# Kernel optimization log

Measured on AMD Instinct MI355X. Metric: run time of the kernel, lower is better.

The kernel has to match this reference:

```python
import jax, jax.numpy as jnp
import numpy as np

N_NODES = 65536   # N
D_HID   = 128     # D (hidden)
N_GROUPS = 16384  # G portfolios
GROUP_LEN = 64    # lines per portfolio (port_len entries)
N_LINES = N_GROUPS * GROUP_LEN  # L
BATCH = 16384     # B samples


def setup_inputs() -> dict:
    key = jax.random.key(0)
    k = jax.random.split(key, 5)
    H = jax.random.normal(k[0], (N_NODES, D_HID), dtype=jnp.float32)
    port_w_signed_flat = jax.random.normal(k[1], (N_LINES,), dtype=jnp.float32)
    anchor_idx = jax.random.randint(k[2], (BATCH,), 0, N_NODES, dtype=jnp.int32)
    pf_gid = jax.random.randint(k[3], (BATCH,), 0, N_GROUPS, dtype=jnp.int32)
    port_nodes_flat = jax.random.randint(k[4], (N_LINES,), 0, N_NODES, dtype=jnp.int32)
    port_len = jnp.full((N_GROUPS,), GROUP_LEN, dtype=jnp.int32)
    return {
        'H': H,
        'port_w_signed_flat': port_w_signed_flat,
        'anchor_idx': anchor_idx,
        'pf_gid': pf_gid,
        'port_nodes_flat': port_nodes_flat,
        'port_len': port_len,
    }


def reference(H, port_w_signed_flat, anchor_idx, pf_gid, port_nodes_flat, port_len):
    """Faithful, vectorized port of compute_samplewise_portfolio_vectors_loo.

    Ragged segment-weighted mean per portfolio group, with strict leave-one-out
    correction for each sample's anchor node, followed by L2 normalization.
    Returns (V_abs, V_sgn), each [B, D].
    """
    N, D = H.shape
    G = port_len.shape[0]
    L = port_nodes_flat.shape[0]

    # gid per flat line: repeat_interleave(arange(G), lens)
    gid_lines = jnp.repeat(jnp.arange(G, dtype=jnp.int32), port_len,
                           total_repeat_length=L)

    w_abs = jnp.abs(port_w_signed_flat)
    Hl = H[port_nodes_flat]                                  # [L, D] gather
    S_abs = jax.ops.segment_sum(w_abs[:, None] * Hl, gid_lines, num_segments=G)
    W_abs = jax.ops.segment_sum(w_abs, gid_lines, num_segments=G)
    W_sgn = jax.ops.segment_sum(port_w_signed_flat, gid_lines, num_segments=G)

    valid = (pf_gid >= 0) & (pf_gid < G)
    g = jnp.clip(pf_gid, 0, G - 1)

    # Leave-one-out self-weight: sum of w over lines where (gid==g_i, node==anchor_i).
    # Vectorized join via a sorted composite int32 key (G*N < 2^31 by construction).
    keys_l = gid_lines * N + port_nodes_flat                 # [L]
    keys_s = g * N + anchor_idx                              # [B]
    order = jnp.argsort(keys_l)
    sk = keys_l[order]
    zero1 = jnp.zeros((1,), H.dtype)
    ca = jnp.concatenate([zero1, jnp.cumsum(w_abs[order])])
    cs = jnp.concatenate([zero1, jnp.cumsum(port_w_signed_flat[order])])
    lo = jnp.searchsorted(sk, keys_s, side='left')
    hi = jnp.searchsorted(sk, keys_s, side='right')
    self_w_abs = ca[hi] - ca[lo]                             # [B]
    self_w_sgn = cs[hi] - cs[lo]                             # [B]

    Ha = H[anchor_idx]                                       # [B, D]
    denom = jnp.maximum(W_abs[g] - self_w_abs, 1e-12)        # clamp_min
    V_abs = (S_abs[g] - self_w_abs[:, None] * Ha) / denom[:, None]
    V_sgn = ((W_sgn[g] - self_w_sgn) / denom)[:, None] * V_abs

    V_abs = jnp.where(valid[:, None], V_abs, jnp.zeros((), H.dtype))
    V_sgn = jnp.where(valid[:, None], V_sgn, jnp.zeros((), H.dtype))

    # torch F.normalize: x / clamp(||x||, min=eps)
    na = jnp.linalg.norm(V_abs, axis=1, keepdims=True)
    V_abs = V_abs / jnp.maximum(na, 1e-6)
    ns = jnp.linalg.norm(V_sgn, axis=1, keepdims=True)
    V_sgn = jnp.where(ns > 0, V_sgn / jnp.maximum(ns, 1e-6), V_sgn)
    return V_abs, V_sgn
```

## Files before the change

kernel.cpp:

```cpp
#include <hip/hip_runtime.h>
#include <hip/hip_bf16.h>


#define DDIM 128

__device__ inline unsigned bf_rne(float x) {
    unsigned u = __float_as_uint(x);
    return (u + 0x7FFFu + ((u >> 16) & 1u)) >> 16;
}

__device__ inline void unpack2(unsigned d, float& lo, float& hi) {
    lo = __uint_as_float(d << 16);
    hi = __uint_as_float(d & 0xFFFF0000u);
}

__global__ __launch_bounds__(1024) void init_kernel(
    const float4* __restrict__ H4, uint2* __restrict__ Hb, int n4,
    const int* __restrict__ plen, int* __restrict__ offs, int G,
    const int* __restrict__ pf_gid, int* __restrict__ used, int B, int nconv) {
    const int t = threadIdx.x;
    const int bb = blockIdx.x;
    if (bb < nconv) {
        const int i = bb * 1024 + t;
        if (i < n4) {
            const float4 v = H4[i];
            uint2 o;
            o.x = bf_rne(v.x) | (bf_rne(v.y) << 16);
            o.y = bf_rne(v.z) | (bf_rne(v.w) << 16);
            Hb[i] = o;
        }
        return;
    }
    if (bb == nconv) {
        for (int i = t; i < G; i += 1024) used[i] = 0;
        __syncthreads();
        for (int i = t; i < B; i += 1024) {
            const int g = pf_gid[i];
            if (g >= 0 && g < G) used[g] = 1;
        }
        return;
    }
    __shared__ int part[1024];
    const int chunk = (G + 1023) >> 10;
    const int lo = min(t * chunk, G);
    const int hi = min(lo + chunk, G);
    int s = 0;
    for (int i = lo; i < hi; ++i) s += plen[i];
    part[t] = s;
    __syncthreads();
    #pragma unroll
    for (int ofs = 1; ofs < 1024; ofs <<= 1) {
        int v = (t >= ofs) ? part[t - ofs] : 0;
        __syncthreads();
        part[t] += v;
        __syncthreads();
    }
    int run = part[t] - s;
    for (int i = lo; i < hi; ++i) { offs[i] = run; run += plen[i]; }
}

__global__ __launch_bounds__(128) void group_sums(
    const unsigned short* __restrict__ Hb,
    const float* __restrict__ pw, const int* __restrict__ pn,
    const int* __restrict__ plen, const int* __restrict__ offs,
    const int* __restrict__ used,
    float* __restrict__ Sabs, float* __restrict__ Wag,
    float* __restrict__ Wsg, int G) {
    const int g = blockIdx.x;
    if (g >= G || !used[g]) return;
    const int tid = threadIdx.x;
    const int wid = tid >> 6;
    const int lane = tid & 63;
    const int q = lane >> 4;
    const int s = lane & 15;

    __shared__ float ldsS[2][DDIM];
    __shared__ float ldsW[4];

    const int off = offs[g];
    const int len = plen[g];

    float acc[8] = {0.f, 0.f, 0.f, 0.f, 0.f, 0.f, 0.f, 0.f};
    float laWa = 0.f, laWs = 0.f;

    for (int base = 0; base < len; base += 64) {
        const int l0 = base + wid * 32;
        float wl = 0.f;
        int nl = 0;
        if (lane < 32 && l0 + lane < len) {
            wl = pw[off + l0 + lane];
            nl = pn[off + l0 + lane];
        }
        laWa += fabsf(wl);
        laWs += wl;

        #pragma unroll
        for (int jj = 0; jj < 32; jj += 4) {
            const float ww = fabsf(__shfl(wl, jj + q));
            const int row = __shfl(nl, jj + q);
            const uint4 h = *((const uint4*)(Hb + (size_t)row * DDIM) + s);
            float f0, f1, f2, f3, f4, f5, f6, f7;
            unpack2(h.x, f0, f1);
            unpack2(h.y, f2, f3);
            unpack2(h.z, f4, f5);
            unpack2(h.w, f6, f7);
            acc[0] = fmaf(ww, f0, acc[0]);
            acc[1] = fmaf(ww, f1, acc[1]);
            acc[2] = fmaf(ww, f2, acc[2]);
            acc[3] = fmaf(ww, f3, acc[3]);
            acc[4] = fmaf(ww, f4, acc[4]);
            acc[5] = fmaf(ww, f5, acc[5]);
            acc[6] = fmaf(ww, f6, acc[6]);
            acc[7] = fmaf(ww, f7, acc[7]);
        }
    }

    #pragma unroll
    for (int m = 32; m; m >>= 1) {
        laWa += __shfl_xor(laWa, m);
        laWs += __shfl_xor(laWs, m);
    }
    #pragma unroll
    for (int k = 0; k < 8; ++k) {
        acc[k] += __shfl_xor(acc[k], 16);
        acc[k] += __shfl_xor(acc[k], 32);
    }

    if (q == 0) {
        #pragma unroll
        for (int k = 0; k < 8; ++k) ldsS[wid][8 * s + k] = acc[k];
    }
    if (lane == 0) { ldsW[wid] = laWa; ldsW[2 + wid] = laWs; }
    __syncthreads();

    if (tid < DDIM) {
        Sabs[(size_t)g * DDIM + tid] = ldsS[0][tid] + ldsS[1][tid];
    }
    if (tid == 0) {
        Wag[g] = ldsW[0] + ldsW[1];
        Wsg[g] = ldsW[2] + ldsW[3];
    }
}

__global__ __launch_bounds__(256) void per_sample(
    const unsigned short* __restrict__ Hb,
    const float* __restrict__ pw, const int* __restrict__ pn,
    const int* __restrict__ plen, const int* __restrict__ offs,
    const float* __restrict__ Sabs, const float* __restrict__ Wag,
    const float* __restrict__ Wsg,
    const int* __restrict__ anchor_idx, const int* __restrict__ pf_gid,
    float* __restrict__ out, int B, int G) {
    const int b = blockIdx.x * (blockDim.x >> 6) + (threadIdx.x >> 6);
    const int lane = threadIdx.x & 63;
    if (b >= B) return;

    float2* outA = (float2*)(out + (size_t)b * DDIM);
    float2* outS = (float2*)(out + ((size_t)B + b) * DDIM);

    const int g = pf_gid[b];
    if (!(g >= 0 && g < G)) {
        const float2 z = make_float2(0.f, 0.f);
        outA[lane] = z;
        outS[lane] = z;
        return;
    }

    const int anchor = anchor_idx[b];
    const int off = offs[g];
    const int len = plen[g];

    float selfa = 0.f, selfs = 0.f;
    for (int base = 0; base < len; base += 64) {
        const int jmax = min(64, len - base);
        if (lane < jmax) {
            const float w = pw[off + base + lane];
            const int n = pn[off + base + lane];
            if (n == anchor) { selfa += fabsf(w); selfs += w; }
        }
    }
    #pragma unroll
    for (int m = 32; m; m >>= 1) {
        selfa += __shfl_xor(selfa, m);
        selfs += __shfl_xor(selfs, m);
    }

    const float Wa = Wag[g];
    const float Wsn = Wsg[g];
    const float2 S = ((const float2*)(Sabs + (size_t)g * DDIM))[lane];
    const unsigned hb = *((const unsigned*)(Hb + (size_t)anchor * DDIM) + lane);
    float h0, h1;
    unpack2(hb, h0, h1);

    const float denom = fmaxf(Wa - selfa, 1e-12f);
    float2 v;
    v.x = (S.x - selfa * h0) / denom;
    v.y = (S.y - selfa * h1) / denom;
    const float scale = (Wsn - selfs) / denom;

    float n2 = v.x * v.x + v.y * v.y;
    #pragma unroll
    for (int m = 32; m; m >>= 1) n2 += __shfl_xor(n2, m);
    const float na = sqrtf(n2);

    const float invA = 1.0f / fmaxf(na, 1e-6f);
    const float ns = fabsf(scale) * na;
    const float sgnscale = (ns > 0.f) ? (scale / fmaxf(ns, 1e-6f)) : scale;

    outA[lane] = make_float2(v.x * invA, v.y * invA);
    outS[lane] = make_float2(v.x * sgnscale, v.y * sgnscale);
}

__global__ __launch_bounds__(1024) void scan_only(
    const int* __restrict__ len, int* __restrict__ offs, int G) {
    __shared__ int part[1024];
    const int t = threadIdx.x;
    const int chunk = (G + 1023) >> 10;
    const int lo = min(t * chunk, G);
    const int hi = min(lo + chunk, G);
    int s = 0;
    for (int i = lo; i < hi; ++i) s += len[i];
    part[t] = s;
    __syncthreads();
    #pragma unroll
    for (int ofs = 1; ofs < 1024; ofs <<= 1) {
        int v = (t >= ofs) ? part[t - ofs] : 0;
        __syncthreads();
        part[t] += v;
        __syncthreads();
    }
    int run = part[t] - s;
    for (int i = lo; i < hi; ++i) { offs[i] = run; run += len[i]; }
}

__global__ __launch_bounds__(256) void pf_loo_f32(
    const float* __restrict__ H, const float* __restrict__ pw,
    const int* __restrict__ anchor_idx, const int* __restrict__ pf_gid,
    const int* __restrict__ pn, const int* __restrict__ plen,
    const int* __restrict__ offs, float* __restrict__ out, int B, int G) {
    const int b = blockIdx.x * (blockDim.x >> 6) + (threadIdx.x >> 6);
    const int lane = threadIdx.x & 63;
    const int half = lane >> 5;
    const int qlane = lane & 31;
    if (b >= B) return;
    float4* outA = (float4*)(out + (size_t)b * DDIM);
    float4* outS = (float4*)(out + ((size_t)B + b) * DDIM);
    const int gid = pf_gid[b];
    if (!(gid >= 0 && gid < G)) {
        float4 z = make_float4(0.f, 0.f, 0.f, 0.f);
        if (half == 0) { outA[qlane] = z; outS[qlane] = z; }
        return;
    }
    const int anchor = anchor_idx[b];
    const int off = offs[gid];
    const int len = plen[gid];
    float4 acc = make_float4(0.f, 0.f, 0.f, 0.f);
    float laWa = 0.f, laWs = 0.f, laSa = 0.f, laSs = 0.f;
    for (int base = 0; base < len; base += 64) {
        const int jmax = min(64, len - base);
        float wl = 0.f;
        int nl = -1;
        if (lane < jmax) { wl = pw[off + base + lane]; nl = pn[off + base + lane]; }
        const float wla = fabsf(wl);
        laWa += wla; laWs += wl;
        if (nl == anchor) { laSa += wla; laSs += wl; }
        #pragma unroll 8
        for (int jj = 0; jj < 64; jj += 2) {
            const float ww = fabsf(__shfl(wl, jj + half));
            const int row = __shfl(nl, jj + half);
            const float4 h = ((const float4*)(H + (size_t)row * DDIM))[qlane];
            acc.x = fmaf(ww, h.x, acc.x);
            acc.y = fmaf(ww, h.y, acc.y);
            acc.z = fmaf(ww, h.z, acc.z);
            acc.w = fmaf(ww, h.w, acc.w);
        }
    }
    #pragma unroll
    for (int m = 32; m; m >>= 1) {
        laWa += __shfl_xor(laWa, m);
        laWs += __shfl_xor(laWs, m);
        laSa += __shfl_xor(laSa, m);
        laSs += __shfl_xor(laSs, m);
    }
    acc.x += __shfl_xor(acc.x, 32);
    acc.y += __shfl_xor(acc.y, 32);
    acc.z += __shfl_xor(acc.z, 32);
    acc.w += __shfl_xor(acc.w, 32);
    const float denom = fmaxf(laWa - laSa, 1e-12f);
    const float4 hv = ((const float4*)(H + (size_t)anchor * DDIM))[qlane];
    float4 v;
    v.x = (acc.x - laSa * hv.x) / denom;
    v.y = (acc.y - laSa * hv.y) / denom;
    v.z = (acc.z - laSa * hv.z) / denom;
    v.w = (acc.w - laSa * hv.w) / denom;
    const float scale = (laWs - laSs) / denom;
    float n2 = v.x * v.x + v.y * v.y + v.z * v.z + v.w * v.w;
    #pragma unroll
    for (int m = 32; m; m >>= 1) n2 += __shfl_xor(n2, m);
    n2 *= 0.5f;
    const float na = sqrtf(n2);
    const float invA = 1.0f / fmaxf(na, 1e-6f);
    const float ns = fabsf(scale) * na;
    const float sgnscale = (ns > 0.f) ? (scale / fmaxf(ns, 1e-6f)) : scale;
    const float sc = half ? sgnscale : invA;
    float4 res = make_float4(v.x * sc, v.y * sc, v.z * sc, v.w * sc);
    float4* dst = half ? outS : outA;
    dst[qlane] = res;
}

extern "C" void kernel_launch(void* const* d_in, const int* in_sizes, int n_in,
                              void* d_out, int out_size, void* d_ws, size_t ws_size,
                              hipStream_t stream) {
    const float* H      = (const float*)d_in[0];
    const float* pw     = (const float*)d_in[1];
    const int* anchor   = (const int*)d_in[2];
    const int* gid      = (const int*)d_in[3];
    const int* pn       = (const int*)d_in[4];
    const int* plen     = (const int*)d_in[5];
    float* out          = (float*)d_out;

    const int B = in_sizes[2];
    const int G = in_sizes[5];
    const int ND = in_sizes[0];
    const size_t hb_bytes = (size_t)ND * 2;
    const size_t sabs_bytes = (size_t)G * DDIM * 4;
    const size_t need = hb_bytes + sabs_bytes + (size_t)G * 4 * 4;

    if (ws_size >= need) {
        char* p = (char*)d_ws;
        unsigned short* Hb = (unsigned short*)p;        p += hb_bytes;
        float* Sabs        = (float*)p;                 p += sabs_bytes;
        int* offsp         = (int*)p;                   p += (size_t)G * 4;
        int* usedp         = (int*)p;                   p += (size_t)G * 4;
        float* Wag         = (float*)p;                 p += (size_t)G * 4;
        float* Wsg         = (float*)p;

        const int n4 = ND / 4;
        const int nconv = (n4 + 1023) / 1024;
        init_kernel<<<nconv + 2, 1024, 0, stream>>>(
            (const float4*)H, (uint2*)Hb, n4, plen, offsp, G, gid, usedp, B, nconv);

        group_sums<<<G, 128, 0, stream>>>(Hb, pw, pn, plen, offsp, usedp,
                                          Sabs, Wag, Wsg, G);

        const int sblocks = (B + 3) / 4;
        per_sample<<<sblocks, 256, 0, stream>>>(Hb, pw, pn, plen, offsp, Sabs,
                                                Wag, Wsg, anchor, gid, out, B, G);
    } else {
        int* offsp = (int*)d_ws;
        scan_only<<<1, 1024, 0, stream>>>(plen, offsp, G);
        const int blocks = (B + 3) / 4;
        pf_loo_f32<<<blocks, 256, 0, stream>>>(H, pw, anchor, gid, pn, plen,
                                               offsp, out, B, G);
    }
}
```

Before: 142.9 us.

## Compute each group sum with one wavefront instead of a two-wave block

```diff
diff --git a/kernel.cpp b/kernel.cpp
--- a/kernel.cpp
+++ b/kernel.cpp
@@ -59,24 +59,20 @@
     for (int i = lo; i < hi; ++i) { offs[i] = run; run += plen[i]; }
 }
 
-__global__ __launch_bounds__(128) void group_sums(
+__global__ __launch_bounds__(256) void group_sums(
     const unsigned short* __restrict__ Hb,
     const float* __restrict__ pw, const int* __restrict__ pn,
     const int* __restrict__ plen, const int* __restrict__ offs,
     const int* __restrict__ used,
     float* __restrict__ Sabs, float* __restrict__ Wag,
     float* __restrict__ Wsg, int G) {
-    const int g = blockIdx.x;
-    if (g >= G || !used[g]) return;
-    const int tid = threadIdx.x;
-    const int wid = tid >> 6;
-    const int lane = tid & 63;
+    const int g = blockIdx.x * 4 + (threadIdx.x >> 6);
+    if (g >= G) return;
+    if (!used[g]) return;
+    const int lane = threadIdx.x & 63;
     const int q = lane >> 4;
     const int s = lane & 15;
 
-    __shared__ float ldsS[2][DDIM];
-    __shared__ float ldsW[4];
-
     const int off = offs[g];
     const int len = plen[g];
 
@@ -84,18 +80,17 @@
     float laWa = 0.f, laWs = 0.f;
 
     for (int base = 0; base < len; base += 64) {
-        const int l0 = base + wid * 32;
         float wl = 0.f;
         int nl = 0;
-        if (lane < 32 && l0 + lane < len) {
-            wl = pw[off + l0 + lane];
-            nl = pn[off + l0 + lane];
+        if (base + lane < len) {
+            wl = pw[off + base + lane];
+            nl = pn[off + base + lane];
         }
         laWa += fabsf(wl);
         laWs += wl;
 
         #pragma unroll
-        for (int jj = 0; jj < 32; jj += 4) {
+        for (int jj = 0; jj < 64; jj += 4) {
             const float ww = fabsf(__shfl(wl, jj + q));
             const int row = __shfl(nl, jj + q);
             const uint4 h = *((const uint4*)(Hb + (size_t)row * DDIM) + s);
@@ -127,19 +122,11 @@
     }
 
     if (q == 0) {
-        #pragma unroll
-        for (int k = 0; k < 8; ++k) ldsS[wid][8 * s + k] = acc[k];
-    }
-    if (lane == 0) { ldsW[wid] = laWa; ldsW[2 + wid] = laWs; }
-    __syncthreads();
-
-    if (tid < DDIM) {
-        Sabs[(size_t)g * DDIM + tid] = ldsS[0][tid] + ldsS[1][tid];
-    }
-    if (tid == 0) {
-        Wag[g] = ldsW[0] + ldsW[1];
-        Wsg[g] = ldsW[2] + ldsW[3];
-    }
+        float4* dst = (float4*)(Sabs + (size_t)g * DDIM + 8 * s);
+        dst[0] = make_float4(acc[0], acc[1], acc[2], acc[3]);
+        dst[1] = make_float4(acc[4], acc[5], acc[6], acc[7]);
+    }
+    if (lane == 0) { Wag[g] = laWa; Wsg[g] = laWs; }
 }
 
 __global__ __launch_bounds__(256) void per_sample(
@@ -339,8 +326,9 @@
         init_kernel<<<nconv + 2, 1024, 0, stream>>>(
             (const float4*)H, (uint2*)Hb, n4, plen, offsp, G, gid, usedp, B, nconv);
 
-        group_sums<<<G, 128, 0, stream>>>(Hb, pw, pn, plen, offsp, usedp,
-                                          Sabs, Wag, Wsg, G);
+        const int gblocks = (G + 3) / 4;
+        group_sums<<<gblocks, 256, 0, stream>>>(Hb, pw, pn, plen, offsp, usedp,
+                                                Sabs, Wag, Wsg, G);
 
         const int sblocks = (B + 3) / 4;
         per_sample<<<sblocks, 256, 0, stream>>>(Hb, pw, pn, plen, offsp, Sabs,
```

After: 141.7 us (median of 2 runs). No clear change (-0.8%).
